# Performance work log

Measured on AMD Instinct MI355X. Metric: run time of the kernel, lower is better.

Reference implementation:

```python
import jax, jax.numpy as jnp
import numpy as np

N, E, IN, HID, OUT, B = 50000, 800000, 128, 128, 64, 4096
EPS = 1e-5


def setup_inputs() -> dict:
    key = jax.random.key(0)
    ks = jax.random.split(key, 12)
    x = jax.random.normal(ks[0], (N, IN), jnp.float32)
    edge_index = jax.random.randint(ks[1], (2, E), 0, N, dtype=jnp.int32).astype(jnp.int64)
    target_index = jax.random.randint(ks[2], (B,), 0, N, dtype=jnp.int32).astype(jnp.int64)

    def lin(k, i, o):
        return jax.random.normal(k, (i, o), jnp.float32) * (1.0 / np.sqrt(i))

    return {
        'x': x, 'edge_index': edge_index, 'target_index': target_index,
        'W0': lin(ks[3], IN, HID), 'b0': jnp.zeros((HID,), jnp.float32),
        'W1': lin(ks[4], HID, HID), 'b1': jnp.zeros((HID,), jnp.float32),
        'W2': lin(ks[5], HID, HID), 'b2': jnp.zeros((HID,), jnp.float32),
        'g0': jnp.ones((HID,), jnp.float32), 'bt0': jnp.zeros((HID,), jnp.float32),
        'g1': jnp.ones((HID,), jnp.float32), 'bt1': jnp.zeros((HID,), jnp.float32),
        'f1w': lin(ks[6], HID, HID), 'f1b': jnp.zeros((HID,), jnp.float32),
        'f2w': lin(ks[7], HID, OUT), 'f2b': jnp.zeros((OUT,), jnp.float32),
    }


def _gcn_layer(h, W, b, src, dst, norm):
    # GCNConv: D^-1/2 (A+I) D^-1/2 (h W) + b  (self-loops already in src/dst)
    h = h @ W                                        # [N, out]
    msg = h[src] * norm[:, None]                     # [E+N, out]
    return jax.ops.segment_sum(msg, dst, num_segments=N) + b


def _batchnorm(h, g, bt):
    mu = jnp.mean(h, axis=0)
    var = jnp.mean((h - mu) ** 2, axis=0)            # biased, as torch BN
    return g * (h - mu) * jax.lax.rsqrt(var + EPS) + bt


def reference(x, edge_index, target_index, W0, b0, W1, b1, W2, b2,
              g0, bt0, g1, bt1, f1w, f1b, f2w, f2b):
    loop = jnp.arange(N, dtype=edge_index.dtype)
    src = jnp.concatenate([edge_index[0], loop])
    dst = jnp.concatenate([edge_index[1], loop])
    deg = jax.ops.segment_sum(jnp.ones_like(dst, jnp.float32), dst, num_segments=N)
    dinv = jax.lax.rsqrt(deg)                        # deg >= 1 via self-loops
    norm = dinv[src] * dinv[dst]                     # [E+N]

    h = _gcn_layer(x, W0, b0, src, dst, norm)
    h = jax.nn.relu(_batchnorm(h, g0, bt0))
    h = _gcn_layer(h, W1, b1, src, dst, norm)
    h = jax.nn.relu(_batchnorm(h, g1, bt1))
    h = _gcn_layer(h, W2, b2, src, dst, norm)

    # target_index.unsqueeze(1).expand(-1,-1) -> [B,1]; pool squeezes dim 1
    t = h[target_index]                              # [B, HID]
    t = jax.nn.relu(t @ f1w + f1b)                   # FeedForwardNetwork layer1 (dropout=0)
    return t @ f2w + f2b                             # [B, OUT]
```

## Files before the change

kernel.cpp:

```cpp
#include <hip/hip_runtime.h>


static const int GNN5566_NN  = 50000;
static const int GNN5566_NE  = 800000;
static const int GNN5566_NB  = 4096;
static const int GNN5566_CAP = 64;

static const int GNN5566_NBUCK  = (GNN5566_NN + 63) / 64;
static const int GNN5566_NCHUNK = 256;
static const int GNN5566_CHUNK  = GNN5566_NE / GNN5566_NCHUNK;

static const int GNN5566_WSLOT = 17408;

typedef short gnn5566_s16x8 __attribute__((ext_vector_type(8)));
typedef float gnn5566_f32x4 __attribute__((ext_vector_type(4)));

static __device__ inline float gnn5566_b2f(unsigned short h){
  return __uint_as_float(((unsigned int)h) << 16);
}
static __device__ inline unsigned short gnn5566_f2b(float f){
  unsigned int u = __float_as_uint(f);
  u += 0x7fffu + ((u >> 16) & 1u);
  return (unsigned short)(u >> 16);
}
static __device__ inline float gnn5566_loadf(const void* p, long long i, int isF32){
  if (isF32) return ((const float*)p)[i];
  return gnn5566_b2f(((const unsigned short*)p)[i]);
}

__global__ void GNNEncoder_5566277616090_wprep(const void* W0, const void* W1,
                                               const void* W2, const void* f1w,
                                               const void* f2w, unsigned short* wT,
                                               const int* ei, const int* tgt,
                                               int* flags, int* done){
  __shared__ unsigned short lt[128][129];
  __shared__ int sF32;
  int b = blockIdx.x, tid = threadIdx.x;

  if (b == 5) {
    if (tid < 8) done[tid] = 0;
    if (tid < 64) {
      int o1 = ei[2*tid + 1];
      int o2 = tgt[2*tid + 1];
      unsigned int w = ((const unsigned int*)W0)[tid];
      unsigned int e = (w >> 7) & 255u;
      unsigned long long m1 = __ballot(o1 != 0);
      unsigned long long m2 = __ballot(o2 != 0);
      unsigned long long m3 = __ballot(e >= 96u && e <= 134u);
      if (tid == 0) {
        flags[0] = (m1 == 0ull) ? 1 : 0;
        flags[1] = (m2 == 0ull) ? 1 : 0;
        flags[2] = (__popcll(m3) >= 56) ? 0 : 1;
      }
    }
    return;
  }

  if (tid < 64) {
    unsigned int w = ((const unsigned int*)W0)[tid];
    unsigned int e = (w >> 7) & 255u;
    unsigned long long m3 = __ballot(e >= 96u && e <= 134u);
    if (tid == 0) sF32 = (__popcll(m3) >= 56) ? 0 : 1;
  }
  __syncthreads();
  int f32 = sF32;

  const void* src = (b == 0) ? W0 : (b == 1) ? W1 : (b == 2) ? W2
                  : (b == 3) ? f1w : f2w;
  int wide = (b != 4);
  int tot = wide ? 16384 : 8192;
  for (int i = tid; i < tot; i += 256) {
    int k = wide ? (i >> 7) : (i >> 6);
    int c = wide ? (i & 127) : (i & 63);
    lt[k][c] = f32 ? gnn5566_f2b(((const float*)src)[i])
                   : ((const unsigned short*)src)[i];
  }
  __syncthreads();
  unsigned short* out = wT + b * GNN5566_WSLOT;
  int wtot = wide ? 2048 : 1024;
  for (int j = tid; j < wtot; j += 256) {
    int c = j >> 4, k8 = (j & 15) << 3;
    unsigned int p0 = (unsigned int)lt[k8    ][c] | ((unsigned int)lt[k8 + 1][c] << 16);
    unsigned int p1 = (unsigned int)lt[k8 + 2][c] | ((unsigned int)lt[k8 + 3][c] << 16);
    unsigned int p2 = (unsigned int)lt[k8 + 4][c] | ((unsigned int)lt[k8 + 5][c] << 16);
    unsigned int p3 = (unsigned int)lt[k8 + 6][c] | ((unsigned int)lt[k8 + 7][c] << 16);
    uint4 v; v.x = p0; v.y = p1; v.z = p2; v.w = p3;
    *(uint4*)(out + c * 136 + k8) = v;
  }
}

__global__ void GNNEncoder_5566277616090_fillH(const int* ei, unsigned int* histT,
                                               const int* flags){
  __shared__ int h[GNN5566_NBUCK];
  int tid = threadIdx.x, chunk = blockIdx.x;
  for (int b = tid; b < GNN5566_NBUCK; b += 256) h[b] = 0;
  __syncthreads();
  int f = flags[0];
  int base = chunk * GNN5566_CHUNK;
  for (int i = tid; i < GNN5566_CHUNK; i += 256) {
    int e = base + i;
    int d = f ? ((const int2*)ei)[GNN5566_NE + e].x : ei[GNN5566_NE + e];
    atomicAdd(&h[d >> 6], 1);
  }
  __syncthreads();
  for (int b = tid; b < GNN5566_NBUCK; b += 256)
    histT[b * GNN5566_NCHUNK + chunk] = (unsigned int)h[b];
}

__global__ void GNNEncoder_5566277616090_fillS1(unsigned int* histT, int* btot,
                                                int* segStart, int* doneCtr){
  __shared__ int sv[256];
  __shared__ int lastFlag;
  int tid  = threadIdx.x;
  int wv   = (int)(blockIdx.x * 4u + (tid >> 6));
  int lane = tid & 63;

  if (wv < GNN5566_NBUCK) {
    unsigned int* row = histT + wv * GNN5566_NCHUNK;
    uint4 v = ((const uint4*)row)[lane];
    int a = (int)v.x, b = (int)v.y, c = (int)v.z, d = (int)v.w;
    int s = a + b + c + d;
    int incl = s;
    #pragma unroll
    for (int off = 1; off < 64; off <<= 1) {
      int t = __shfl_up(incl, off, 64);
      if (lane >= off) incl += t;
    }
    int excl = incl - s;
    uint4 o;
    o.x = (unsigned int)excl;
    o.y = (unsigned int)(excl + a);
    o.z = (unsigned int)(excl + a + b);
    o.w = (unsigned int)(excl + a + b + c);
    ((uint4*)row)[lane] = o;
    if (lane == 63) atomicExch(&btot[wv], incl);
  }
  __syncthreads();
  if (tid == 0) {
    __threadfence();
    lastFlag = (atomicAdd(doneCtr, 1) == (int)gridDim.x - 1);
  }
  __syncthreads();
  if (!lastFlag) return;

  int i0 = tid * 4;
  int v0 = (i0     < GNN5566_NBUCK) ? atomicAdd(&btot[i0    ], 0) : 0;
  int v1 = (i0 + 1 < GNN5566_NBUCK) ? atomicAdd(&btot[i0 + 1], 0) : 0;
  int v2 = (i0 + 2 < GNN5566_NBUCK) ? atomicAdd(&btot[i0 + 2], 0) : 0;
  int v3 = (i0 + 3 < GNN5566_NBUCK) ? atomicAdd(&btot[i0 + 3], 0) : 0;
  int t01 = v0 + v1, t012 = t01 + v2, T = t012 + v3;
  sv[tid] = T;
  __syncthreads();
  for (int off = 1; off < 256; off <<= 1) {
    int add = (tid >= off) ? sv[tid - off] : 0;
    __syncthreads();
    sv[tid] += add;
    __syncthreads();
  }
  int excl = sv[tid] - T;
  if (i0     < GNN5566_NBUCK) segStart[i0]     = excl;
  if (i0 + 1 < GNN5566_NBUCK) segStart[i0 + 1] = excl + v0;
  if (i0 + 2 < GNN5566_NBUCK) segStart[i0 + 2] = excl + t01;
  if (i0 + 3 < GNN5566_NBUCK) segStart[i0 + 3] = excl + t012;
  if (tid == 0) segStart[GNN5566_NBUCK] = GNN5566_NE;
}

__global__ void GNNEncoder_5566277616090_fillScatter(const int* ei,
                                                     const unsigned int* histT,
                                                     const int* segStart,
                                                     unsigned int* sorted,
                                                     const int* flags){
  __shared__ int cur[GNN5566_NBUCK];
  int tid = threadIdx.x, chunk = blockIdx.x;
  for (int b = tid; b < GNN5566_NBUCK; b += 256)
    cur[b] = (int)histT[b * GNN5566_NCHUNK + chunk] + segStart[b];
  __syncthreads();
  int f = flags[0];
  int base = chunk * GNN5566_CHUNK;
  for (int i = tid; i < GNN5566_CHUNK; i += 256) {
    int e = base + i;
    int s = f ? ((const int2*)ei)[e].x                : ei[e];
    int d = f ? ((const int2*)ei)[GNN5566_NE + e].x   : ei[GNN5566_NE + e];
    int p = atomicAdd(&cur[d >> 6], 1);
    sorted[p] = ((unsigned int)s << 6) | (unsigned int)(d & 63);
  }
}

__global__ void GNNEncoder_5566277616090_fillB(const int* segStart,
                                               const unsigned int* sorted,
                                               unsigned short* colIdx16, int* cnt,
                                               float* dinv){
  __shared__ unsigned int lbuf[64 * 32];
  __shared__ int lcnt[64];
  int b   = blockIdx.x;
  int tid = threadIdx.x;
  if (tid < 64) lcnt[tid] = 0;
  __syncthreads();

  int s0 = segStart[b];
  int n  = segStart[b + 1] - s0;
  const unsigned int* bp = sorted + s0;
  unsigned short* lists = (unsigned short*)lbuf;
  for (int i = tid; i < n; i += 256) {
    unsigned int w = bp[i];
    int d = (int)(w & 63u);
    int s = (int)(w >> 6);
    int p = atomicAdd(&lcnt[d], 1);
    if (p < GNN5566_CAP) lists[d * 64 + p] = (unsigned short)s;
  }
  __syncthreads();

  if (tid < 64) {
    int node = b * 64 + tid;
    if (node < GNN5566_NN) {
      int c = lcnt[tid];
      cnt[node]  = c;
      dinv[node] = rsqrtf((float)(c + 1));
    }
  }
  unsigned int* out = (unsigned int*)colIdx16;
  for (int idx = tid; idx < 2048; idx += 256) {
    int d = idx >> 5;
    int node = b * 64 + d;
    if (node < GNN5566_NN)
      out[(long long)node * 32 + (idx & 31)] = lbuf[idx];
  }
}

__global__ void GNNEncoder_5566277616090_kernel(const void* A,
                                                const unsigned short* wT,
                                                unsigned short* Out, int nRows,
                                                const float* bnA, const float* bnC,
                                                const float* rowScale,
                                                const void* bias, int reluOut,
                                                int aExternal, const int* flags)
{
  __shared__ __align__(16) unsigned short gnnLw[128 * 136];
  __shared__ float lbnA[128], lbnC[128], lbias[128];
  int tid = threadIdx.x;
  int wF32 = flags[2];
  int aF32 = aExternal ? wF32 : 0;

  {
    const uint4* src = (const uint4*)wT;
    uint4* dst = (uint4*)gnnLw;
    for (int i = tid; i < 2176; i += 256) dst[i] = src[i];
  }
  if (tid < 128) {
    lbnA[tid]  = bnA  ? bnA[tid] : 0.0f;
    lbnC[tid]  = bnC  ? bnC[tid] : 0.0f;
    lbias[tid] = bias ? gnn5566_loadf(bias, tid, wF32) : 0.0f;
  }
  __syncthreads();

  int wave = tid >> 6, lane = tid & 63;
  int q = lane >> 4, ln = lane & 15;
  int rowBase = blockIdx.x * 64 + wave * 16;
  int r  = rowBase + ln;
  int cr = (r < nRows) ? r : (nRows - 1);
  float rs = rowScale ? rowScale[cr] : 1.0f;
  int useBN = (bnA != 0);

  gnn5566_s16x8 afr[4];
  #pragma unroll
  for (int kk = 0; kk < 4; ++kk) {
    int kb = kk * 32 + q * 8;
    float vals[8];
    if (aF32) {
      const float4* ap = (const float4*)A + (long long)cr * 32 + (kb >> 2);
      float4 u = ap[0], w = ap[1];
      vals[0] = u.x; vals[1] = u.y; vals[2] = u.z; vals[3] = u.w;
      vals[4] = w.x; vals[5] = w.y; vals[6] = w.z; vals[7] = w.w;
    } else {
      const uint4* ap = (const uint4*)A + (long long)cr * 16 + (kb >> 3);
      uint4 u = ap[0];
      vals[0] = gnn5566_b2f((unsigned short)(u.x & 0xffffu));
      vals[1] = gnn5566_b2f((unsigned short)(u.x >> 16));
      vals[2] = gnn5566_b2f((unsigned short)(u.y & 0xffffu));
      vals[3] = gnn5566_b2f((unsigned short)(u.y >> 16));
      vals[4] = gnn5566_b2f((unsigned short)(u.z & 0xffffu));
      vals[5] = gnn5566_b2f((unsigned short)(u.z >> 16));
      vals[6] = gnn5566_b2f((unsigned short)(u.w & 0xffffu));
      vals[7] = gnn5566_b2f((unsigned short)(u.w >> 16));
    }
    if (useBN) {
      float4 a0 = *(const float4*)&lbnA[kb], a1 = *(const float4*)&lbnA[kb + 4];
      float4 c0 = *(const float4*)&lbnC[kb], c1 = *(const float4*)&lbnC[kb + 4];
      vals[0] = fmaxf(vals[0] * a0.x + c0.x, 0.0f);
      vals[1] = fmaxf(vals[1] * a0.y + c0.y, 0.0f);
      vals[2] = fmaxf(vals[2] * a0.z + c0.z, 0.0f);
      vals[3] = fmaxf(vals[3] * a0.w + c0.w, 0.0f);
      vals[4] = fmaxf(vals[4] * a1.x + c1.x, 0.0f);
      vals[5] = fmaxf(vals[5] * a1.y + c1.y, 0.0f);
      vals[6] = fmaxf(vals[6] * a1.z + c1.z, 0.0f);
      vals[7] = fmaxf(vals[7] * a1.w + c1.w, 0.0f);
    }
    #pragma unroll
    for (int j = 0; j < 8; ++j) afr[kk][j] = (short)gnn5566_f2b(vals[j] * rs);
  }

  gnn5566_f32x4 zero4;
  zero4[0] = 0.0f; zero4[1] = 0.0f; zero4[2] = 0.0f; zero4[3] = 0.0f;
  gnn5566_f32x4 acc[8];
  #pragma unroll
  for (int t = 0; t < 8; ++t) acc[t] = zero4;

  #pragma unroll
  for (int kk = 0; kk < 4; ++kk) {
    int kb = kk * 32 + q * 8;
    #pragma unroll
    for (int t = 0; t < 8; ++t) {
      gnn5566_s16x8 bfr = *(const gnn5566_s16x8*)(&gnnLw[(t * 16 + ln) * 136 + kb]);
      acc[t] = __builtin_amdgcn_mfma_f32_16x16x32_bf16(afr[kk], bfr, acc[t], 0, 0, 0);
    }
  }

  __syncthreads();
  #pragma unroll
  for (int t = 0; t < 8; ++t) {
    int col = t * 16 + ln;
    float badd = lbias[col];
    #pragma unroll
    for (int rg = 0; rg < 4; ++rg) {
      float v = acc[t][rg] + badd;
      if (reluOut) v = fmaxf(v, 0.0f);
      gnnLw[(wave * 16 + q * 4 + rg) * 136 + col] = gnn5566_f2b(v);
    }
  }
  __syncthreads();
  int tRowBase = blockIdx.x * 64;
  for (int j = tid; j < 1024; j += 256) {
    int rr = j >> 4, c4 = j & 15;
    int grow = tRowBase + rr;
    if (grow < nRows) {
      uint4 v = *(const uint4*)&gnnLw[rr * 136 + c4 * 8];
      *(uint4*)&Out[(long long)grow * 128 + c4 * 8] = v;
    }
  }
}

__global__ void GNNEncoder_5566277616090_ffn(const unsigned short* A,
                                             const unsigned short* wT3,
                                             const unsigned short* wT4,
                                             void* Out, const int* tgt,
                                             const int* tgtFlag,
                                             const void* f1b, const void* fb2,
                                             const int* flags)
{
  __shared__ __align__(16) unsigned short lwA[128 * 136];
  __shared__ __align__(16) unsigned short lwB[64 * 136];
  __shared__ __align__(16) unsigned short ep[64 * 136];
  __shared__ float lb1[128];
  __shared__ float lb2[64];
  int tid = threadIdx.x;
  int f32 = flags[2];

  {
    const uint4* sA = (const uint4*)wT3;
    uint4* dA = (uint4*)lwA;
    for (int i = tid; i < 2176; i += 256) dA[i] = sA[i];
    const uint4* sB = (const uint4*)wT4;
    uint4* dB = (uint4*)lwB;
    for (int i = tid; i < 1088; i += 256) dB[i] = sB[i];
  }
  if (tid < 128) lb1[tid] = gnn5566_loadf(f1b, tid, f32);
  if (tid < 64)  lb2[tid] = gnn5566_loadf(fb2, tid, f32);
  __syncthreads();

  int wave = tid >> 6, lane = tid & 63;
  int q = lane >> 4, ln = lane & 15;
  int rowBase = blockIdx.x * 64 + wave * 16;
  int r  = rowBase + ln;
  int cr = (r < GNN5566_NB) ? r : (GNN5566_NB - 1);
  int ar = (*tgtFlag) ? tgt[2 * cr] : tgt[cr];

  gnn5566_s16x8 afr[4];
  #pragma unroll
  for (int kk = 0; kk < 4; ++kk) {
    int kb = kk * 32 + q * 8;
    const uint4* ap = (const uint4*)A + (long long)ar * 16 + (kb >> 3);
    uint4 u = ap[0];
    unsigned short e[8];
    e[0] = (unsigned short)(u.x & 0xffffu); e[1] = (unsigned short)(u.x >> 16);
    e[2] = (unsigned short)(u.y & 0xffffu); e[3] = (unsigned short)(u.y >> 16);
    e[4] = (unsigned short)(u.z & 0xffffu); e[5] = (unsigned short)(u.z >> 16);
    e[6] = (unsigned short)(u.w & 0xffffu); e[7] = (unsigned short)(u.w >> 16);
    #pragma unroll
    for (int j = 0; j < 8; ++j) afr[kk][j] = (short)e[j];
  }

  gnn5566_f32x4 zero4;
  zero4[0] = 0.0f; zero4[1] = 0.0f; zero4[2] = 0.0f; zero4[3] = 0.0f;
  gnn5566_f32x4 acc[8];
  #pragma unroll
  for (int t = 0; t < 8; ++t) acc[t] = zero4;
  #pragma unroll
  for (int kk = 0; kk < 4; ++kk) {
    int kb = kk * 32 + q * 8;
    #pragma unroll
    for (int t = 0; t < 8; ++t) {
      gnn5566_s16x8 bfr = *(const gnn5566_s16x8*)(&lwA[(t * 16 + ln) * 136 + kb]);
      acc[t] = __builtin_amdgcn_mfma_f32_16x16x32_bf16(afr[kk], bfr, acc[t], 0, 0, 0);
    }
  }
  #pragma unroll
  for (int t = 0; t < 8; ++t) {
    int col = t * 16 + ln;
    float badd = lb1[col];
    #pragma unroll
    for (int rg = 0; rg < 4; ++rg) {
      float v = fmaxf(acc[t][rg] + badd, 0.0f);
      ep[(wave * 16 + q * 4 + rg) * 136 + col] = gnn5566_f2b(v);
    }
  }
  __syncthreads();

  gnn5566_s16x8 afr2[4];
  #pragma unroll
  for (int kk = 0; kk < 4; ++kk) {
    int kb = kk * 32 + q * 8;
    afr2[kk] = *(const gnn5566_s16x8*)(&ep[(wave * 16 + ln) * 136 + kb]);
  }
  gnn5566_f32x4 acc2[4];
  #pragma unroll
  for (int t = 0; t < 4; ++t) acc2[t] = zero4;
  #pragma unroll
  for (int kk = 0; kk < 4; ++kk) {
    int kb = kk * 32 + q * 8;
    #pragma unroll
    for (int t = 0; t < 4; ++t) {
      gnn5566_s16x8 bfr = *(const gnn5566_s16x8*)(&lwB[(t * 16 + ln) * 136 + kb]);
      acc2[t] = __builtin_amdgcn_mfma_f32_16x16x32_bf16(afr2[kk], bfr, acc2[t], 0, 0, 0);
    }
  }
  #pragma unroll
  for (int t = 0; t < 4; ++t) {
    int col = t * 16 + ln;
    float badd = lb2[col];
    #pragma unroll
    for (int rg = 0; rg < 4; ++rg) {
      int grow = rowBase + q * 4 + rg;
      if (grow < GNN5566_NB) {
        float v = acc2[t][rg] + badd;
        if (f32) ((float*)Out)[(long long)grow * 64 + col] = v;
        else     ((unsigned short*)Out)[(long long)grow * 64 + col] = gnn5566_f2b(v);
      }
    }
  }
}

__global__ void GNNEncoder_5566277616090_agg(const unsigned short* hs,
                                             const unsigned short* colIdx16,
                                             const int* cnt, const float* dinv,
                                             const void* bias, unsigned short* ha,
                                             const int* flags)
{
  int gw = (int)((blockIdx.x * 256u + threadIdx.x) >> 6);
  if (gw >= GNN5566_NN) return;
  int lane = threadIdx.x & 63;
  const unsigned int* hrow = (const unsigned int*)hs;
  unsigned int sv = hrow[(long long)gw * 64 + lane];
  float a0 = __uint_as_float(sv << 16);
  float a1 = __uint_as_float(sv & 0xffff0000u);
  int m = cnt[gw]; if (m > GNN5566_CAP) m = GNN5566_CAP;
  const unsigned short* cp = colIdx16 + (long long)gw * GNN5566_CAP;
  const uint4* cp4 = (const uint4*)cp;
  int i = 0;
  for (; i + 8 <= m; i += 8) {
    uint4 iw = cp4[i >> 3];
    unsigned int s0 = iw.x & 0xffffu, s1 = iw.x >> 16;
    unsigned int s2 = iw.y & 0xffffu, s3 = iw.y >> 16;
    unsigned int s4 = iw.z & 0xffffu, s5 = iw.z >> 16;
    unsigned int s6 = iw.w & 0xffffu, s7 = iw.w >> 16;
    unsigned int v0 = hrow[(long long)s0 * 64 + lane];
    unsigned int v1 = hrow[(long long)s1 * 64 + lane];
    unsigned int v2 = hrow[(long long)s2 * 64 + lane];
    unsigned int v3 = hrow[(long long)s3 * 64 + lane];
    unsigned int v4 = hrow[(long long)s4 * 64 + lane];
    unsigned int v5 = hrow[(long long)s5 * 64 + lane];
    unsigned int v6 = hrow[(long long)s6 * 64 + lane];
    unsigned int v7 = hrow[(long long)s7 * 64 + lane];
    a0 += __uint_as_float(v0 << 16) + __uint_as_float(v1 << 16)
        + __uint_as_float(v2 << 16) + __uint_as_float(v3 << 16)
        + __uint_as_float(v4 << 16) + __uint_as_float(v5 << 16)
        + __uint_as_float(v6 << 16) + __uint_as_float(v7 << 16);
    a1 += __uint_as_float(v0 & 0xffff0000u) + __uint_as_float(v1 & 0xffff0000u)
        + __uint_as_float(v2 & 0xffff0000u) + __uint_as_float(v3 & 0xffff0000u)
        + __uint_as_float(v4 & 0xffff0000u) + __uint_as_float(v5 & 0xffff0000u)
        + __uint_as_float(v6 & 0xffff0000u) + __uint_as_float(v7 & 0xffff0000u);
  }
  for (; i < m; ++i) {
    unsigned int v = hrow[(long long)cp[i] * 64 + lane];
    a0 += __uint_as_float(v << 16);
    a1 += __uint_as_float(v & 0xffff0000u);
  }
  float s = dinv[gw];
  int f32 = flags[2];
  float o0 = a0 * s + gnn5566_loadf(bias, lane * 2,     f32);
  float o1 = a1 * s + gnn5566_loadf(bias, lane * 2 + 1, f32);
  unsigned int packed = (unsigned int)gnn5566_f2b(o0)
                      | (((unsigned int)gnn5566_f2b(o1)) << 16);
  ((unsigned int*)ha)[(long long)gw * 64 + lane] = packed;
}

__global__ void GNNEncoder_5566277616090_stats(const unsigned short* ha, float* partial,
                                               const void* g, const void* bt,
                                               float* bnA, float* bnC,
                                               const int* flags, int* doneCtr){
  __shared__ float red[256];
  __shared__ int lastFlag;
  const unsigned int* h32 = (const unsigned int*)ha;
  int tid = threadIdx.x;
  int cp2 = tid & 63, sub = tid >> 6;
  float s0 = 0.0f, s1 = 0.0f, q0 = 0.0f, q1 = 0.0f;
  for (int r = blockIdx.x * 4 + sub; r < GNN5566_NN; r += 512) {
    unsigned int v = h32[(long long)r * 64 + cp2];
    float a = __uint_as_float(v << 16);
    float b = __uint_as_float(v & 0xffff0000u);
    s0 += a; q0 += a * a; s1 += b; q1 += b * b;
  }
  float* prow = partial + blockIdx.x * 256;
  red[tid] = s0; __syncthreads();
  if (sub == 0) atomicExch(&prow[2*cp2],
      red[cp2] + red[64+cp2] + red[128+cp2] + red[192+cp2]);
  __syncthreads();
  red[tid] = s1; __syncthreads();
  if (sub == 0) atomicExch(&prow[2*cp2 + 1],
      red[cp2] + red[64+cp2] + red[128+cp2] + red[192+cp2]);
  __syncthreads();
  red[tid] = q0; __syncthreads();
  if (sub == 0) atomicExch(&prow[128 + 2*cp2],
      red[cp2] + red[64+cp2] + red[128+cp2] + red[192+cp2]);
  __syncthreads();
  red[tid] = q1; __syncthreads();
  if (sub == 0) atomicExch(&prow[128 + 2*cp2 + 1],
      red[cp2] + red[64+cp2] + red[128+cp2] + red[192+cp2]);
  __syncthreads();

  if (tid == 0) {
    __threadfence();
    lastFlag = (atomicAdd(doneCtr, 1) == (int)gridDim.x - 1);
  }
  __syncthreads();
  if (!lastFlag) return;

  float acc = 0.0f;
  for (int b = 0; b < (int)gridDim.x; b += 8) {
    float p0 = atomicAdd(&partial[(b    ) * 256 + tid], 0.0f);
    float p1 = atomicAdd(&partial[(b + 1) * 256 + tid], 0.0f);
    float p2 = atomicAdd(&partial[(b + 2) * 256 + tid], 0.0f);
    float p3 = atomicAdd(&partial[(b + 3) * 256 + tid], 0.0f);
    float p4 = atomicAdd(&partial[(b + 4) * 256 + tid], 0.0f);
    float p5 = atomicAdd(&partial[(b + 5) * 256 + tid], 0.0f);
    float p6 = atomicAdd(&partial[(b + 6) * 256 + tid], 0.0f);
    float p7 = atomicAdd(&partial[(b + 7) * 256 + tid], 0.0f);
    acc += ((p0 + p1) + (p2 + p3)) + ((p4 + p5) + (p6 + p7));
  }
  red[tid] = acc;
  __syncthreads();
  if (tid < 128) {
    int f32 = flags[2];
    float invN = 1.0f / (float)GNN5566_NN;
    float mu  = red[tid] * invN;
    float var = red[128 + tid] * invN - mu * mu;
    if (var < 0.0f) var = 0.0f;
    float a = gnn5566_loadf(g, tid, f32) * rsqrtf(var + 1e-5f);
    bnA[tid] = a;
    bnC[tid] = gnn5566_loadf(bt, tid, f32) - mu * a;
  }
}

extern "C" void kernel_launch(void* const* d_in, const int* in_sizes, int n_in,
                              void* d_out, int out_size, void* d_ws, size_t ws_size,
                              hipStream_t stream)
{
  const void* x   = d_in[0];
  const int*  ei  = (const int*)d_in[1];
  const int*  tgt = (const int*)d_in[2];
  const void* W0  = d_in[3];
  const void* b0  = d_in[4];
  const void* W1  = d_in[5];
  const void* b1  = d_in[6];
  const void* W2  = d_in[7];
  const void* b2  = d_in[8];
  const void* g0  = d_in[9];
  const void* bt0 = d_in[10];
  const void* g1  = d_in[11];
  const void* bt1 = d_in[12];
  const void* f1w = d_in[13];
  const void* f1b = d_in[14];
  const void* f2w = d_in[15];
  const void* fb2 = d_in[16];

  char* ws = (char*)d_ws;
  int*            segStart = (int*)           (ws + 0);
  int*            btot     = (int*)           (ws + 4096);
  int*            cnt      = (int*)           (ws + 8192);
  float*          dinv     = (float*)         (ws + 208896);
  unsigned short* wT       = (unsigned short*)(ws + 409600);
  unsigned int*   histT    = (unsigned int*)  (ws + 583936);
  unsigned int*   sorted   = (unsigned int*)  (ws + 1384960);
  unsigned short* colIdx16 = (unsigned short*)(ws + 4585216);
  unsigned short* hs       = (unsigned short*)(ws + 10985472);
  unsigned short* ha       = (unsigned short*)(ws + 23785728);
  float*          partial  = (float*)         (ws + 36585984);
  float*          bn       = (float*)         (ws + 36848128);
  int*            flags    = (int*)           (ws + 36850176);
  int*            done     = (int*)           (ws + 36850432);

  float* bn0A = bn;       float* bn0C = bn + 128;
  float* bn1A = bn + 256; float* bn1C = bn + 384;

  GNNEncoder_5566277616090_wprep <<<6, 256, 0, stream>>>(
      W0, W1, W2, f1w, f2w, wT, ei, tgt, flags, done);
  GNNEncoder_5566277616090_fillH <<<GNN5566_NCHUNK, 256, 0, stream>>>(ei, histT, flags);
  GNNEncoder_5566277616090_fillS1<<<196, 256, 0, stream>>>(histT, btot, segStart, done);
  GNNEncoder_5566277616090_fillScatter<<<GNN5566_NCHUNK, 256, 0, stream>>>(
      ei, histT, segStart, sorted, flags);
  GNNEncoder_5566277616090_fillB <<<GNN5566_NBUCK, 256, 0, stream>>>(
      segStart, sorted, colIdx16, cnt, dinv);

  const int gemmGrid = (GNN5566_NN + 63) / 64;

  GNNEncoder_5566277616090_kernel<<<gemmGrid, 256, 0, stream>>>(
      x, wT, hs, GNN5566_NN, (const float*)0, (const float*)0, dinv,
      (const void*)0, 0, 1, flags);
  GNNEncoder_5566277616090_agg  <<<12500, 256, 0, stream>>>(hs, colIdx16, cnt, dinv, b0, ha, flags);
  GNNEncoder_5566277616090_stats<<<128, 256, 0, stream>>>(
      ha, partial, g0, bt0, bn0A, bn0C, flags, done + 1);

  GNNEncoder_5566277616090_kernel<<<gemmGrid, 256, 0, stream>>>(
      ha, wT + GNN5566_WSLOT, hs, GNN5566_NN, bn0A, bn0C, dinv,
      (const void*)0, 0, 0, flags);
  GNNEncoder_5566277616090_agg  <<<12500, 256, 0, stream>>>(hs, colIdx16, cnt, dinv, b1, ha, flags);
  GNNEncoder_5566277616090_stats<<<128, 256, 0, stream>>>(
      ha, partial + 32768, g1, bt1, bn1A, bn1C, flags, done + 2);

  GNNEncoder_5566277616090_kernel<<<gemmGrid, 256, 0, stream>>>(
      ha, wT + 2 * GNN5566_WSLOT, hs, GNN5566_NN, bn1A, bn1C, dinv,
      (const void*)0, 0, 0, flags);
  GNNEncoder_5566277616090_agg  <<<12500, 256, 0, stream>>>(hs, colIdx16, cnt, dinv, b2, ha, flags);

  GNNEncoder_5566277616090_ffn<<<64, 256, 0, stream>>>(
      ha, wT + 3 * GNN5566_WSLOT, wT + 4 * GNN5566_WSLOT, d_out,
      tgt, flags + 1, f1b, fb2, flags);
}
```

Measured before the change: 376.2 us.

## Merge weight prep with edge histogram, cut chunk count, prefetch A rows, unroll gather

Fuses the weight-transpose kernel and the destination-bucket histogram kernel into one launch, with each block computing its own index-format flag instead of reading it from the flags buffer. It also reduces the edge chunk count from 256 to 64, which simplifies the per-bucket scan to one element per lane. The GEMM kernel now issues its A-row global loads before staging weights into shared memory so the two latencies overlap. The aggregation loop adds a 16-wide unrolled gather for more memory-level parallelism. Fewer chunks mean fewer blocks in the histogram and scatter stages, which may lower their parallelism.

Result: no change. 374.1 us (-0.6%).

```diff
diff --git a/kernel.cpp b/kernel.cpp
--- a/kernel.cpp
+++ b/kernel.cpp
@@ -7,7 +7,7 @@
 static const int GNN5566_CAP = 64;
 
 static const int GNN5566_NBUCK  = (GNN5566_NN + 63) / 64;
-static const int GNN5566_NCHUNK = 256;
+static const int GNN5566_NCHUNK = 64;
 static const int GNN5566_CHUNK  = GNN5566_NE / GNN5566_NCHUNK;
 
 static const int GNN5566_WSLOT = 17408;
@@ -28,16 +28,18 @@
   return gnn5566_b2f(((const unsigned short*)p)[i]);
 }
 
-__global__ void GNNEncoder_5566277616090_wprep(const void* W0, const void* W1,
-                                               const void* W2, const void* f1w,
-                                               const void* f2w, unsigned short* wT,
-                                               const int* ei, const int* tgt,
-                                               int* flags, int* done){
+__global__ void GNNEncoder_5566277616090_prep(const void* W0, const void* W1,
+                                              const void* W2, const void* f1w,
+                                              const void* f2w, unsigned short* wT,
+                                              const int* ei, const int* tgt,
+                                              int* flags, int* done,
+                                              unsigned int* histT){
   __shared__ unsigned short lt[128][129];
-  __shared__ int sF32;
+  __shared__ int h[GNN5566_NBUCK];
+  __shared__ int sFlag;
   int b = blockIdx.x, tid = threadIdx.x;
 
-  if (b == 5) {
+  if (b == 69) {
     if (tid < 8) done[tid] = 0;
     if (tid < 64) {
       int o1 = ei[2*tid + 1];
@@ -56,55 +58,58 @@
     return;
   }
 
+  if (b >= 64) {
+    if (tid < 64) {
+      unsigned int w = ((const unsigned int*)W0)[tid];
+      unsigned int e = (w >> 7) & 255u;
+      unsigned long long m3 = __ballot(e >= 96u && e <= 134u);
+      if (tid == 0) sFlag = (__popcll(m3) >= 56) ? 0 : 1;
+    }
+    __syncthreads();
+    int f32 = sFlag;
+    int slot = b - 64;
+    const void* src = (slot == 0) ? W0 : (slot == 1) ? W1 : (slot == 2) ? W2
+                    : (slot == 3) ? f1w : f2w;
+    int wide = (slot != 4);
+    int tot = wide ? 16384 : 8192;
+    for (int i = tid; i < tot; i += 256) {
+      int k = wide ? (i >> 7) : (i >> 6);
+      int c = wide ? (i & 127) : (i & 63);
+      lt[k][c] = f32 ? gnn5566_f2b(((const float*)src)[i])
+                     : ((const unsigned short*)src)[i];
+    }
+    __syncthreads();
+    unsigned short* out = wT + slot * GNN5566_WSLOT;
+    int wtot = wide ? 2048 : 1024;
+    for (int j = tid; j < wtot; j += 256) {
+      int c = j >> 4, k8 = (j & 15) << 3;
+      unsigned int p0 = (unsigned int)lt[k8    ][c] | ((unsigned int)lt[k8+1][c] << 16);
+      unsigned int p1 = (unsigned int)lt[k8 + 2][c] | ((unsigned int)lt[k8+3][c] << 16);
+      unsigned int p2 = (unsigned int)lt[k8 + 4][c] | ((unsigned int)lt[k8+5][c] << 16);
+      unsigned int p3 = (unsigned int)lt[k8 + 6][c] | ((unsigned int)lt[k8+7][c] << 16);
+      uint4 v; v.x = p0; v.y = p1; v.z = p2; v.w = p3;
+      *(uint4*)(out + c * 136 + k8) = v;
+    }
+    return;
+  }
+
   if (tid < 64) {
-    unsigned int w = ((const unsigned int*)W0)[tid];
-    unsigned int e = (w >> 7) & 255u;
-    unsigned long long m3 = __ballot(e >= 96u && e <= 134u);
-    if (tid == 0) sF32 = (__popcll(m3) >= 56) ? 0 : 1;
-  }
-  __syncthreads();
-  int f32 = sF32;
-
-  const void* src = (b == 0) ? W0 : (b == 1) ? W1 : (b == 2) ? W2
-                  : (b == 3) ? f1w : f2w;
-  int wide = (b != 4);
-  int tot = wide ? 16384 : 8192;
-  for (int i = tid; i < tot; i += 256) {
-    int k = wide ? (i >> 7) : (i >> 6);
-    int c = wide ? (i & 127) : (i & 63);
-    lt[k][c] = f32 ? gnn5566_f2b(((const float*)src)[i])
-                   : ((const unsigned short*)src)[i];
-  }
-  __syncthreads();
-  unsigned short* out = wT + b * GNN5566_WSLOT;
-  int wtot = wide ? 2048 : 1024;
-  for (int j = tid; j < wtot; j += 256) {
-    int c = j >> 4, k8 = (j & 15) << 3;
-    unsigned int p0 = (unsigned int)lt[k8    ][c] | ((unsigned int)lt[k8 + 1][c] << 16);
-    unsigned int p1 = (unsigned int)lt[k8 + 2][c] | ((unsigned int)lt[k8 + 3][c] << 16);
-    unsigned int p2 = (unsigned int)lt[k8 + 4][c] | ((unsigned int)lt[k8 + 5][c] << 16);
-    unsigned int p3 = (unsigned int)lt[k8 + 6][c] | ((unsigned int)lt[k8 + 7][c] << 16);
-    uint4 v; v.x = p0; v.y = p1; v.z = p2; v.w = p3;
-    *(uint4*)(out + c * 136 + k8) = v;
-  }
-}
-
-__global__ void GNNEncoder_5566277616090_fillH(const int* ei, unsigned int* histT,
-                                               const int* flags){
-  __shared__ int h[GNN5566_NBUCK];
-  int tid = threadIdx.x, chunk = blockIdx.x;
-  for (int b = tid; b < GNN5566_NBUCK; b += 256) h[b] = 0;
-  __syncthreads();
-  int f = flags[0];
-  int base = chunk * GNN5566_CHUNK;
+    int o1 = ei[2*tid + 1];
+    unsigned long long m1 = __ballot(o1 != 0);
+    if (tid == 0) sFlag = (m1 == 0ull) ? 1 : 0;
+  }
+  for (int i = tid; i < GNN5566_NBUCK; i += 256) h[i] = 0;
+  __syncthreads();
+  int f = sFlag;
+  int base = b * GNN5566_CHUNK;
   for (int i = tid; i < GNN5566_CHUNK; i += 256) {
     int e = base + i;
     int d = f ? ((const int2*)ei)[GNN5566_NE + e].x : ei[GNN5566_NE + e];
     atomicAdd(&h[d >> 6], 1);
   }
   __syncthreads();
-  for (int b = tid; b < GNN5566_NBUCK; b += 256)
-    histT[b * GNN5566_NCHUNK + chunk] = (unsigned int)h[b];
+  for (int i = tid; i < GNN5566_NBUCK; i += 256)
+    histT[i * GNN5566_NCHUNK + b] = (unsigned int)h[i];
 }
 
 __global__ void GNNEncoder_5566277616090_fillS1(unsigned int* histT, int* btot,
@@ -117,22 +122,14 @@
 
   if (wv < GNN5566_NBUCK) {
     unsigned int* row = histT + wv * GNN5566_NCHUNK;
-    uint4 v = ((const uint4*)row)[lane];
-    int a = (int)v.x, b = (int)v.y, c = (int)v.z, d = (int)v.w;
-    int s = a + b + c + d;
+    int s = (int)row[lane];
     int incl = s;
     #pragma unroll
     for (int off = 1; off < 64; off <<= 1) {
       int t = __shfl_up(incl, off, 64);
       if (lane >= off) incl += t;
     }
-    int excl = incl - s;
-    uint4 o;
-    o.x = (unsigned int)excl;
-    o.y = (unsigned int)(excl + a);
-    o.z = (unsigned int)(excl + a + b);
-    o.w = (unsigned int)(excl + a + b + c);
-    ((uint4*)row)[lane] = o;
+    row[lane] = (unsigned int)(incl - s);
     if (lane == 63) atomicExch(&btot[wv], incl);
   }
   __syncthreads();
@@ -241,18 +238,6 @@
   int wF32 = flags[2];
   int aF32 = aExternal ? wF32 : 0;
 
-  {
-    const uint4* src = (const uint4*)wT;
-    uint4* dst = (uint4*)gnnLw;
-    for (int i = tid; i < 2176; i += 256) dst[i] = src[i];
-  }
-  if (tid < 128) {
-    lbnA[tid]  = bnA  ? bnA[tid] : 0.0f;
-    lbnC[tid]  = bnC  ? bnC[tid] : 0.0f;
-    lbias[tid] = bias ? gnn5566_loadf(bias, tid, wF32) : 0.0f;
-  }
-  __syncthreads();
-
   int wave = tid >> 6, lane = tid & 63;
   int q = lane >> 4, ln = lane & 15;
   int rowBase = blockIdx.x * 64 + wave * 16;
@@ -261,19 +246,41 @@
   float rs = rowScale ? rowScale[cr] : 1.0f;
   int useBN = (bnA != 0);
 
+  uint4  rawU[4];
+  float4 rawF[8];
+  if (aF32) {
+    const float4* ap = (const float4*)A + (long long)cr * 32 + q * 2;
+    #pragma unroll
+    for (int kk = 0; kk < 4; ++kk) { rawF[2*kk] = ap[kk*8]; rawF[2*kk+1] = ap[kk*8+1]; }
+  } else {
+    const uint4* ap = (const uint4*)A + (long long)cr * 16 + q;
+    #pragma unroll
+    for (int kk = 0; kk < 4; ++kk) rawU[kk] = ap[kk * 4];
+  }
+
+  {
+    const uint4* src = (const uint4*)wT;
+    uint4* dst = (uint4*)gnnLw;
+    for (int i = tid; i < 2176; i += 256) dst[i] = src[i];
+  }
+  if (tid < 128) {
+    lbnA[tid]  = bnA  ? bnA[tid] : 0.0f;
+    lbnC[tid]  = bnC  ? bnC[tid] : 0.0f;
+    lbias[tid] = bias ? gnn5566_loadf(bias, tid, wF32) : 0.0f;
+  }
+  __syncthreads();
+
   gnn5566_s16x8 afr[4];
   #pragma unroll
   for (int kk = 0; kk < 4; ++kk) {
     int kb = kk * 32 + q * 8;
     float vals[8];
     if (aF32) {
-      const float4* ap = (const float4*)A + (long long)cr * 32 + (kb >> 2);
-      float4 u = ap[0], w = ap[1];
+      float4 u = rawF[2*kk], w = rawF[2*kk+1];
       vals[0] = u.x; vals[1] = u.y; vals[2] = u.z; vals[3] = u.w;
       vals[4] = w.x; vals[5] = w.y; vals[6] = w.z; vals[7] = w.w;
     } else {
-      const uint4* ap = (const uint4*)A + (long long)cr * 16 + (kb >> 3);
-      uint4 u = ap[0];
+      uint4 u = rawU[kk];
       vals[0] = gnn5566_b2f((unsigned short)(u.x & 0xffffu));
       vals[1] = gnn5566_b2f((unsigned short)(u.x >> 16));
       vals[2] = gnn5566_b2f((unsigned short)(u.y & 0xffffu));
@@ -466,20 +473,52 @@
   const unsigned short* cp = colIdx16 + (long long)gw * GNN5566_CAP;
   const uint4* cp4 = (const uint4*)cp;
   int i = 0;
+  for (; i + 16 <= m; i += 16) {
+    uint4 iwA = cp4[i >> 3];
+    uint4 iwB = cp4[(i >> 3) + 1];
+    unsigned int v0  = hrow[(long long)(iwA.x & 0xffffu) * 64 + lane];
+    unsigned int v1  = hrow[(long long)(iwA.x >> 16)     * 64 + lane];
+    unsigned int v2  = hrow[(long long)(iwA.y & 0xffffu) * 64 + lane];
+    unsigned int v3  = hrow[(long long)(iwA.y >> 16)     * 64 + lane];
+    unsigned int v4  = hrow[(long long)(iwA.z & 0xffffu) * 64 + lane];
+    unsigned int v5  = hrow[(long long)(iwA.z >> 16)     * 64 + lane];
+    unsigned int v6  = hrow[(long long)(iwA.w & 0xffffu) * 64 + lane];
+    unsigned int v7  = hrow[(long long)(iwA.w >> 16)     * 64 + lane];
+    unsigned int v8  = hrow[(long long)(iwB.x & 0xffffu) * 64 + lane];
+    unsigned int v9  = hrow[(long long)(iwB.x >> 16)     * 64 + lane];
+    unsigned int v10 = hrow[(long long)(iwB.y & 0xffffu) * 64 + lane];
+    unsigned int v11 = hrow[(long long)(iwB.y >> 16)     * 64 + lane];
+    unsigned int v12 = hrow[(long long)(iwB.z & 0xffffu) * 64 + lane];
+    unsigned int v13 = hrow[(long long)(iwB.z >> 16)     * 64 + lane];
+    unsigned int v14 = hrow[(long long)(iwB.w & 0xffffu) * 64 + lane];
+    unsigned int v15 = hrow[(long long)(iwB.w >> 16)     * 64 + lane];
+    a0 += __uint_as_float(v0  << 16) + __uint_as_float(v1  << 16)
+        + __uint_as_float(v2  << 16) + __uint_as_float(v3  << 16)
+        + __uint_as_float(v4  << 16) + __uint_as_float(v5  << 16)
+        + __uint_as_float(v6  << 16) + __uint_as_float(v7  << 16)
+        + __uint_as_float(v8  << 16) + __uint_as_float(v9  << 16)
+        + __uint_as_float(v10 << 16) + __uint_as_float(v11 << 16)
+        + __uint_as_float(v12 << 16) + __uint_as_float(v13 << 16)
+        + __uint_as_float(v14 << 16) + __uint_as_float(v15 << 16);
+    a1 += __uint_as_float(v0  & 0xffff0000u) + __uint_as_float(v1  & 0xffff0000u)
+        + __uint_as_float(v2  & 0xffff0000u) + __uint_as_float(v3  & 0xffff0000u)
+        + __uint_as_float(v4  & 0xffff0000u) + __uint_as_float(v5  & 0xffff0000u)
+        + __uint_as_float(v6  & 0xffff0000u) + __uint_as_float(v7  & 0xffff0000u)
+        + __uint_as_float(v8  & 0xffff0000u) + __uint_as_float(v9  & 0xffff0000u)
+        + __uint_as_float(v10 & 0xffff0000u) + __uint_as_float(v11 & 0xffff0000u)
+        + __uint_as_float(v12 & 0xffff0000u) + __uint_as_float(v13 & 0xffff0000u)
+        + __uint_as_float(v14 & 0xffff0000u) + __uint_as_float(v15 & 0xffff0000u);
+  }
   for (; i + 8 <= m; i += 8) {
     uint4 iw = cp4[i >> 3];
-    unsigned int s0 = iw.x & 0xffffu, s1 = iw.x >> 16;
-    unsigned int s2 = iw.y & 0xffffu, s3 = iw.y >> 16;
-    unsigned int s4 = iw.z & 0xffffu, s5 = iw.z >> 16;
-    unsigned int s6 = iw.w & 0xffffu, s7 = iw.w >> 16;
-    unsigned int v0 = hrow[(long long)s0 * 64 + lane];
-    unsigned int v1 = hrow[(long long)s1 * 64 + lane];
-    unsigned int v2 = hrow[(long long)s2 * 64 + lane];
-    unsigned int v3 = hrow[(long long)s3 * 64 + lane];
-    unsigned int v4 = hrow[(long long)s4 * 64 + lane];
-    unsigned int v5 = hrow[(long long)s5 * 64 + lane];
-    unsigned int v6 = hrow[(long long)s6 * 64 + lane];
-    unsigned int v7 = hrow[(long long)s7 * 64 + lane];
+    unsigned int v0 = hrow[(long long)(iw.x & 0xffffu) * 64 + lane];
+    unsigned int v1 = hrow[(long long)(iw.x >> 16)     * 64 + lane];
+    unsigned int v2 = hrow[(long long)(iw.y & 0xffffu) * 64 + lane];
+    unsigned int v3 = hrow[(long long)(iw.y >> 16)     * 64 + lane];
+    unsigned int v4 = hrow[(long long)(iw.z & 0xffffu) * 64 + lane];
+    unsigned int v5 = hrow[(long long)(iw.z >> 16)     * 64 + lane];
+    unsigned int v6 = hrow[(long long)(iw.w & 0xffffu) * 64 + lane];
+    unsigned int v7 = hrow[(long long)(iw.w >> 16)     * 64 + lane];
     a0 += __uint_as_float(v0 << 16) + __uint_as_float(v1 << 16)
         + __uint_as_float(v2 << 16) + __uint_as_float(v3 << 16)
         + __uint_as_float(v4 << 16) + __uint_as_float(v5 << 16)
@@ -611,9 +650,8 @@
   float* bn0A = bn;       float* bn0C = bn + 128;
   float* bn1A = bn + 256; float* bn1C = bn + 384;
 
-  GNNEncoder_5566277616090_wprep <<<6, 256, 0, stream>>>(
-      W0, W1, W2, f1w, f2w, wT, ei, tgt, flags, done);
-  GNNEncoder_5566277616090_fillH <<<GNN5566_NCHUNK, 256, 0, stream>>>(ei, histT, flags);
+  GNNEncoder_5566277616090_prep  <<<70, 256, 0, stream>>>(
+      W0, W1, W2, f1w, f2w, wT, ei, tgt, flags, done, histT);
   GNNEncoder_5566277616090_fillS1<<<196, 256, 0, stream>>>(histT, btot, segStart, done);
   GNNEncoder_5566277616090_fillScatter<<<GNN5566_NCHUNK, 256, 0, stream>>>(
       ei, histT, segStart, sorted, flags);
```
